# Kernel optimization log

Hardware: AMD Instinct MI355X
Metric: run time of the kernel (lower is better)

Reference implementation:

```python
import jax, jax.numpy as jnp
import numpy as np
import math

H = 512       # hidden_dim
NL = 4        # num_layers
N2 = 32       # d_state // 2
B, L = 8, 4096
DT_MIN, DT_MAX = 1e-3, 1e-1
EPS = 1e-5


def _layer_norm(x, gamma, beta):
    mu = jnp.mean(x, axis=-1, keepdims=True)
    var = jnp.mean(jnp.square(x - mu), axis=-1, keepdims=True)
    return (x - mu) * jax.lax.rsqrt(var + EPS) * gamma + beta


def setup_inputs() -> dict:
    key = jax.random.key(0)
    ks = jax.random.split(key, 8)
    x = jax.random.normal(ks[0], (B, L, H), dtype=jnp.float32)
    # S4DKernel buffers / params, stacked over layers
    log_dt = jax.random.uniform(ks[1], (NL, H)) * (math.log(DT_MAX) - math.log(DT_MIN)) + math.log(DT_MIN)
    A_imag = jnp.broadcast_to(math.pi * jnp.arange(N2, dtype=jnp.float32), (NL, H, N2)).copy()
    log_A_real = jnp.full((NL, H, N2), math.log(0.5), dtype=jnp.float32)
    C = jax.random.normal(ks[2], (NL, H, N2, 2), dtype=jnp.float32)  # view_as_real of cfloat
    D = jax.random.normal(ks[3], (NL, H), dtype=jnp.float32)
    # 1x1 Conv1d h -> 2h (pointwise linear over channels)
    W = jax.random.normal(ks[4], (NL, 2 * H, H), dtype=jnp.float32) / math.sqrt(H)
    b = jax.random.normal(ks[5], (NL, 2 * H), dtype=jnp.float32) * 0.01
    gamma = jnp.ones((NL, H), dtype=jnp.float32)
    beta = jnp.zeros((NL, H), dtype=jnp.float32)
    return dict(x=x, log_dt=log_dt, A_imag=A_imag, log_A_real=log_A_real,
                C=C, D=D, W=W, b=b, gamma=gamma, beta=beta)


def reference(x, log_dt, A_imag, log_A_real, C, D, W, b, gamma, beta):
    Bsz, Lseq, h = x.shape
    t = jnp.arange(Lseq, dtype=jnp.float32)
    for i in range(NL):
        # --- S4D kernel generation ---
        dt = jnp.exp(log_dt[i])                                    # (h,)
        Cc = C[i, ..., 0] + 1j * C[i, ..., 1]                      # (h, n)
        A = -jnp.exp(log_A_real[i]) + 1j * A_imag[i]               # (h, n)
        dA = A * dt[:, None]                                       # (h, n)
        Cmod = Cc * (jnp.exp(dA) - 1.0) / A                        # (h, n)
        # Vandermonde: exp(dA * l), reduced over state dim
        K = 2.0 * jnp.einsum('hn,hnl->hl', Cmod,
                             jnp.exp(dA[:, :, None] * t)).real     # (h, L)
        # --- FFT long convolution ---
        u = jnp.transpose(x, (0, 2, 1))                            # (B, h, L)
        kf = jnp.fft.rfft(K, n=2 * Lseq)                           # (h, L+1)
        uf = jnp.fft.rfft(u, n=2 * Lseq)                           # (B, h, L+1)
        y = jnp.fft.irfft(uf * kf, n=2 * Lseq)[..., :Lseq]         # (B, h, L)
        y = y + u * D[i][:, None]
        y = jax.nn.gelu(y, approximate=False)                      # torch nn.GELU default (erf)
        # 1x1 conv h -> 2h then GLU over channel dim
        z = jnp.einsum('oh,bhl->bol', W[i], y) + b[i][None, :, None]
        a, g = jnp.split(z, 2, axis=1)
        y = a * jax.nn.sigmoid(g)                                  # (B, h, L)
        y = jnp.transpose(y, (0, 2, 1))                            # (B, L, h)
        x = _layer_norm(y + x, gamma[i], beta[i])
    return x
```

## Files before the change

kernel.cpp:

```cpp
#include <hip/hip_runtime.h>
#include <hip/hip_bf16.h>
#include <math.h>

#define H 512
#define NL 4
#define N2 32
#define Bsz 8
#define Lseq 4096
#define BT (Bsz*Lseq)
#define LC2 64
#define NCC (BT/LC2)
#define CPB (Lseq/LC2)

typedef __attribute__((ext_vector_type(8))) short short8;
typedef __attribute__((ext_vector_type(4))) float float4v;


__device__ __forceinline__ float bf2f(unsigned short u) {
    union { unsigned int i; float f; } x; x.i = ((unsigned int)u) << 16; return x.f;
}
__device__ __forceinline__ unsigned short f2bf(float f) {
    union { float f; unsigned int i; } x; x.f = f;
    unsigned int u = x.i + 0x7fff + ((x.i >> 16) & 1);
    return (unsigned short)(u >> 16);
}
__device__ __forceinline__ uint2 pack4bf(float a, float b, float c, float d) {
    uint2 r;
    r.x = (unsigned)f2bf(a) | ((unsigned)f2bf(b) << 16);
    r.y = (unsigned)f2bf(c) | ((unsigned)f2bf(d) << 16);
    return r;
}
__device__ __forceinline__ void async_copy16(const void* g, void* l) {
    __builtin_amdgcn_global_load_lds(
        (const __attribute__((address_space(1))) void*)g,
        (__attribute__((address_space(3))) void*)l, 16, 0, 0);
}

__global__ void wconv_kernel(const float* __restrict__ W, unsigned short* __restrict__ Wbf) {
    int tid = blockIdx.x * 256 + threadIdx.x;
    Wbf[tid] = f2bf(W[tid]);
}

__global__ void params_kernel(const float* __restrict__ log_dt, const float* __restrict__ A_imag,
                              const float* __restrict__ log_A_real, const float* __restrict__ Cin,
                              float* __restrict__ dA, float* __restrict__ Ct) {
    int tid = blockIdx.x * 256 + threadIdx.x;
    int h = tid % H;
    int n = (tid / H) % N2;
    int layer = tid / (H * N2);
    float dt = expf(log_dt[layer * H + h]);
    int pidx = (layer * H + h) * N2 + n;
    float Are = -expf(log_A_real[pidx]);
    float Aim = A_imag[pidx];
    float dre = Are * dt, dim = Aim * dt;
    float er = expf(dre);
    float lre = er * cosf(dim), lim = er * sinf(dim);
    float nre = lre - 1.0f, nim = lim;
    float inv = 1.0f / (Are * Are + Aim * Aim);
    float tre = (nre * Are + nim * Aim) * inv;
    float tim = (nim * Are - nre * Aim) * inv;
    float Ccre = Cin[pidx * 2], Ccim = Cin[pidx * 2 + 1];
    int oidx = ((layer * N2 + n) * 2) * H + h;
    dA[oidx] = dre;  dA[oidx + H] = dim;
    Ct[oidx] = 2.0f * (Ccre * tre - Ccim * tim);
    Ct[oidx + H] = 2.0f * (Ccre * tim + Ccim * tre);
}

__global__ void kergen_k_kernel(const float* __restrict__ dA, const float* __restrict__ Ct,
                                unsigned short* __restrict__ kmat) {
    int t = blockIdx.x * 256 + threadIdx.x;
    int d = t & 63;
    int h = (t >> 6) & (H - 1);
    int layer = t >> 15;
    float fd = (float)d;
    float sum = 0.f;
    for (int n = 0; n < N2; n++) {
        int base = ((layer * N2 + n) * 2) * H + h;
        float dre = dA[base], dim = dA[base + H];
        float Ctr = Ct[base], Cti = Ct[base + H];
        float e = expf(dre * fd);
        sum += Ctr * e * cosf(dim * fd) - Cti * e * sinf(dim * fd);
    }
    kmat[t] = f2bf(sum);
}

__global__ void kergenW_kernel(const float* __restrict__ dA, unsigned short* __restrict__ Wst, int layer) {
    int t = blockIdx.x * 256 + threadIdx.x;
    int j = t & 63;
    int r = (t >> 6) & 63;
    int h = t >> 12;
    int n = r >> 1;
    int base = ((layer * N2 + n) * 2) * H + h;
    float dre = dA[base], dim = dA[base + H];
    float p = (float)(63 - j);
    float e = expf(dre * p);
    Wst[t] = f2bf((r & 1) ? e * sinf(dim * p) : e * cosf(dim * p));
}

__global__ void kergenV_kernel(const float* __restrict__ dA, const float* __restrict__ Ct,
                               unsigned short* __restrict__ Vl, int layer) {
    int t = blockIdx.x * 256 + threadIdx.x;
    int c2 = t & 63;
    int l = (t >> 6) & 63;
    int h = t >> 12;
    int n = c2 >> 1;
    int base = ((layer * N2 + n) * 2) * H + h;
    float dre = dA[base], dim = dA[base + H];
    float Ctr = Ct[base], Cti = Ct[base + H];
    float q = (float)(l + 1);
    float e = expf(dre * q);
    float ar = e * cosf(dim * q), ai = e * sinf(dim * q);
    float vre = Ctr * ar - Cti * ai;
    float vim = Ctr * ai + Cti * ar;
    Vl[t] = f2bf((c2 & 1) ? -vim : vre);
}

__global__ __launch_bounds__(256) void t1_f32_kernel(const float* __restrict__ xi,
                                                     unsigned short* __restrict__ ut) {
    __shared__ float tile[64][68];
    int bx = blockIdx.x;
    int pt = bx & 511, ht = bx >> 9;
    int p0 = pt * 64, h0 = ht * 64;
    int t = threadIdx.x;
    int jr = t & 15, ib = t >> 4;
#pragma unroll
    for (int pass = 0; pass < 4; pass++) {
        int i = ib + pass * 16;
        float4 v = *(const float4*)(xi + (size_t)(p0 + i) * H + h0 + jr * 4);
        *(float4*)(&tile[i][jr * 4]) = v;
    }
    __syncthreads();
#pragma unroll
    for (int pass = 0; pass < 4; pass++) {
        int i2 = ib + pass * 16;
        int j2 = jr * 4;
        uint2 pk = pack4bf(tile[j2][i2], tile[j2 + 1][i2], tile[j2 + 2][i2], tile[j2 + 3][i2]);
        *(uint2*)(ut + (size_t)(h0 + i2) * BT + p0 + j2) = pk;
    }
}

__global__ __launch_bounds__(256) void ssm_kernel(const unsigned short* __restrict__ ut,
                                                  const unsigned short* __restrict__ kmat,
                                                  const unsigned short* __restrict__ Wst,
                                                  const unsigned short* __restrict__ Vl,
                                                  const float* __restrict__ dA,
                                                  const float* __restrict__ Dp,
                                                  unsigned short* __restrict__ yt, int layer) {
    __shared__ unsigned short T[64][72];
    __shared__ unsigned short Sl[64][72];
    __shared__ unsigned short El[64][72];
    int h = blockIdx.x, b = blockIdx.y;
    int t = threadIdx.x;
    const unsigned short* km = kmat + ((size_t)layer * H + h) * 64;
    {
        int l = t >> 2, j0 = (t & 3) * 16;
#pragma unroll
        for (int g = 0; g < 2; g++) {
            short8 v;
#pragma unroll
            for (int e = 0; e < 8; e++) {
                int j = j0 + g * 8 + e;
                v[e] = (j <= l) ? (short)km[l - j] : (short)0;
            }
            *reinterpret_cast<short8*>(&T[l][j0 + g * 8]) = v;
        }
    }
    int wave = t >> 6, lane = t & 63;
    int r16 = lane & 15, quad = lane >> 4;
    const unsigned short* uh = ut + (size_t)h * BT + (size_t)b * Lseq;
    const unsigned short* wh = Wst + (size_t)h * 64 * 64;
    const unsigned short* vh = Vl + (size_t)h * 64 * 64;

    {
        int cc0 = wave * 16;
        float4v acc[4] = {};
#pragma unroll
        for (int k0 = 0; k0 < 64; k0 += 32) {
            short8 bf = *reinterpret_cast<const short8*>(uh + (size_t)(cc0 + r16) * 64 + k0 + quad * 8);
#pragma unroll
            for (int mt = 0; mt < 4; mt++) {
                short8 af = *reinterpret_cast<const short8*>(wh + (mt * 16 + r16) * 64 + k0 + quad * 8);
                acc[mt] = __builtin_amdgcn_mfma_f32_16x16x32_bf16(af, bf, acc[mt], 0, 0, 0);
            }
        }
        int cc = cc0 + r16;
#pragma unroll
        for (int mt = 0; mt < 4; mt++) {
            uint2 pk = pack4bf(acc[mt][0], acc[mt][1], acc[mt][2], acc[mt][3]);
            *(uint2*)(&Sl[cc][mt * 16 + quad * 4]) = pk;
        }
    }
    __syncthreads();

    if (wave == 0) {
        int r = lane;
        int n = r >> 1;
        int base = ((layer * N2 + n) * 2) * H + h;
        float dre = dA[base], dim = dA[base + H];
        float e = expf(dre * 64.f);
        float Lr = e * cosf(dim * 64.f), Li = e * sinf(dim * 64.f);
        float Ls = (r & 1) ? Li : -Li;
        float s = 0.f;
        for (int c = 0; c < 64; c++) {
            El[c][r] = f2bf(s);
            float p = bf2f(Sl[c][r]);
            float sp = __shfl_xor(s, 1);
            s = fmaf(Lr, s, fmaf(Ls, sp, p));
        }
    }
    __syncthreads();

    {
        int cc0 = wave * 16;
        float4v acc[4] = {};
#pragma unroll
        for (int k0 = 0; k0 < 64; k0 += 32) {
            short8 bf = *reinterpret_cast<const short8*>(uh + (size_t)(cc0 + r16) * 64 + k0 + quad * 8);
#pragma unroll
            for (int mt = 0; mt < 4; mt++) {
                short8 af = *reinterpret_cast<const short8*>(&T[mt * 16 + r16][k0 + quad * 8]);
                acc[mt] = __builtin_amdgcn_mfma_f32_16x16x32_bf16(af, bf, acc[mt], 0, 0, 0);
            }
        }
#pragma unroll
        for (int k0 = 0; k0 < 64; k0 += 32) {
            short8 bf = *reinterpret_cast<const short8*>(&El[cc0 + r16][k0 + quad * 8]);
#pragma unroll
            for (int mt = 0; mt < 4; mt++) {
                short8 af = *reinterpret_cast<const short8*>(vh + (mt * 16 + r16) * 64 + k0 + quad * 8);
                acc[mt] = __builtin_amdgcn_mfma_f32_16x16x32_bf16(af, bf, acc[mt], 0, 0, 0);
            }
        }
        float Dh = Dp[layer * H + h];
        int cc = cc0 + r16;
        unsigned short* yh = yt + (size_t)h * BT + (size_t)b * Lseq;
#pragma unroll
        for (int mt = 0; mt < 4; mt++) {
            size_t p = (size_t)cc * 64 + mt * 16 + quad * 4;
            ushort4 uu = *(const ushort4*)(uh + p);
            float o[4];
#pragma unroll
            for (int r = 0; r < 4; r++) {
                float y = acc[mt][r] + Dh * bf2f(((const unsigned short*)&uu)[r]);
                o[r] = 0.5f * y * (1.0f + erff(y * 0.70710678118654752f));
            }
            *(uint2*)(yh + p) = pack4bf(o[0], o[1], o[2], o[3]);
        }
    }
}

__global__ __launch_bounds__(256) void transpose2_kernel(const unsigned short* __restrict__ yt,
                                                         unsigned short* __restrict__ yb) {
    __shared__ unsigned short tile[64][72];
    int bx = blockIdx.x;
    int pt = bx & 511, ht = bx >> 9;
    int p0 = pt * 64, h0 = ht * 64;
    int t = threadIdx.x;
    int jr = t & 7, ib = t >> 3;
#pragma unroll
    for (int pass = 0; pass < 2; pass++) {
        int i = ib + pass * 32;
        short8 v = *reinterpret_cast<const short8*>(yt + (size_t)(h0 + i) * BT + p0 + jr * 8);
        *reinterpret_cast<short8*>(&tile[i][jr * 8]) = v;
    }
    __syncthreads();
    int pp = t >> 2, hg = t & 3;
    short8 o0, o1;
#pragma unroll
    for (int r = 0; r < 8; r++) o0[r] = (short)tile[hg * 16 + r][pp];
#pragma unroll
    for (int r = 0; r < 8; r++) o1[r] = (short)tile[hg * 16 + 8 + r][pp];
    unsigned short* dst = yb + (size_t)(p0 + pp) * H + h0 + hg * 16;
    *reinterpret_cast<short8*>(dst) = o0;
    *reinterpret_cast<short8*>(dst + 8) = o1;
}

__global__ __launch_bounds__(256) void gemm_glu_kernel(const unsigned short* __restrict__ ybf,
                                                       const unsigned short* __restrict__ Wbf,
                                                       const float* __restrict__ bias,
                                                       unsigned short* __restrict__ yo, int layer) {
    __shared__ unsigned short As[3][128 * 32];
    __shared__ unsigned short Bs[3][128 * 32];
    int tid = threadIdx.x;
    int wave = tid >> 6, lane = tid & 63;
    int wr = wave >> 1, wc = wave & 1;
    int r16 = lane & 15, quad = lane >> 4;
    int m0 = blockIdx.x * 128;
    int o0 = blockIdx.y * 64;
    const unsigned short* Wl = Wbf + (size_t)layer * 2 * H * H;

    int srow = lane >> 2;
    int scol = ((lane & 3) ^ ((srow >> 1) & 3)) * 8;
    const unsigned short* aS0 = ybf + ((size_t)(m0 + wave * 16 + srow)) * H + scol;
    const unsigned short* aS1 = aS0 + (size_t)64 * H;
    const unsigned short* bSA = Wl + ((size_t)(o0 + wave * 16 + srow)) * H + scol;
    const unsigned short* bSG = bSA + (size_t)512 * H;
    const int aoff0 = (wave * 16) * 32;
    const int aoff1 = (64 + wave * 16) * 32;

    int rcol = (quad ^ ((r16 >> 1) & 3)) * 8;

    float4v acc_a[4][2] = {}, acc_g[4][2] = {};

    async_copy16(aS0,      &As[0][aoff0]);
    async_copy16(aS1,      &As[0][aoff1]);
    async_copy16(bSA,      &Bs[0][aoff0]);
    async_copy16(bSG,      &Bs[0][aoff1]);
    async_copy16(aS0 + 32, &As[1][aoff0]);
    async_copy16(aS1 + 32, &As[1][aoff1]);
    async_copy16(bSA + 32, &Bs[1][aoff0]);
    async_copy16(bSG + 32, &Bs[1][aoff1]);
    asm volatile("s_waitcnt vmcnt(4)" ::: "memory");
    __builtin_amdgcn_s_barrier();

#pragma unroll
    for (int ks = 0; ks < 16; ++ks) {
        const int b = ks % 3;
        if (ks < 14) {
            const int nb = (ks + 2) % 3;
            const int kn = (ks + 2) * 32;
            async_copy16(aS0 + kn, &As[nb][aoff0]);
            async_copy16(aS1 + kn, &As[nb][aoff1]);
            async_copy16(bSA + kn, &Bs[nb][aoff0]);
            async_copy16(bSG + kn, &Bs[nb][aoff1]);
        }

        short8 af[4], ba[2], bg[2];
#pragma unroll
        for (int mi = 0; mi < 4; mi++)
            af[mi] = *reinterpret_cast<const short8*>(&As[b][(wr * 64 + mi * 16 + r16) * 32 + rcol]);
#pragma unroll
        for (int ni = 0; ni < 2; ni++) {
            ba[ni] = *reinterpret_cast<const short8*>(&Bs[b][(wc * 32 + ni * 16 + r16) * 32 + rcol]);
            bg[ni] = *reinterpret_cast<const short8*>(&Bs[b][(64 + wc * 32 + ni * 16 + r16) * 32 + rcol]);
        }
#pragma unroll
        for (int mi = 0; mi < 4; mi++)
#pragma unroll
            for (int ni = 0; ni < 2; ni++) {
                acc_a[mi][ni] = __builtin_amdgcn_mfma_f32_16x16x32_bf16(af[mi], ba[ni], acc_a[mi][ni], 0, 0, 0);
                acc_g[mi][ni] = __builtin_amdgcn_mfma_f32_16x16x32_bf16(af[mi], bg[ni], acc_g[mi][ni], 0, 0, 0);
            }

        if (ks < 14) {
            asm volatile("s_waitcnt vmcnt(4) lgkmcnt(0)" ::: "memory");
            __builtin_amdgcn_s_barrier();
        } else if (ks == 14) {
            asm volatile("s_waitcnt vmcnt(0) lgkmcnt(0)" ::: "memory");
            __builtin_amdgcn_s_barrier();
        }
    }

    const float* bl = bias + layer * 2 * H;
#pragma unroll
    for (int ni = 0; ni < 2; ni++) {
        int o = o0 + wc * 32 + ni * 16 + r16;
        float ba_ = bl[o], bg_ = bl[H + o];
#pragma unroll
        for (int mi = 0; mi < 4; mi++)
#pragma unroll
            for (int r = 0; r < 4; r++) {
                int l = m0 + wr * 64 + mi * 16 + quad * 4 + r;
                float av = acc_a[mi][ni][r] + ba_;
                float gv = acc_g[mi][ni][r] + bg_;
                yo[(size_t)l * H + o] = f2bf(av * (1.0f / (1.0f + expf(-gv))));
            }
    }
}

__global__ __launch_bounds__(256) void ln_t_kernel(const unsigned short* __restrict__ yo,
                                                   const float* __restrict__ xf,
                                                   const unsigned short* __restrict__ xb,
                                                   const float* __restrict__ gamma,
                                                   const float* __restrict__ beta,
                                                   unsigned short* __restrict__ xR,
                                                   unsigned short* __restrict__ ut,
                                                   int in_f32, int layer) {
    __shared__ unsigned short tl[64][520];
    int t = threadIdx.x;
    int p0 = blockIdx.x * 64;
    int lane8 = t & 7;
    int rowb = t >> 3;
    const float* gl = gamma + layer * H;
    const float* bl = beta + layer * H;
#pragma unroll
    for (int rr = 0; rr < 2; rr++) {
        int row = rowb + rr * 32;
        size_t gbase = (size_t)(p0 + row) * H;
        float v[64];
        float s = 0.f, s2 = 0.f;
#pragma unroll
        for (int cc = 0; cc < 8; cc++) {
            int h0 = (lane8 + cc * 8) * 8;
            short8 yv = *reinterpret_cast<const short8*>(yo + gbase + h0);
            if (in_f32) {
                float4 x0 = *(const float4*)(xf + gbase + h0);
                float4 x1 = *(const float4*)(xf + gbase + h0 + 4);
                v[cc * 8 + 0] = bf2f((unsigned short)yv[0]) + x0.x;
                v[cc * 8 + 1] = bf2f((unsigned short)yv[1]) + x0.y;
                v[cc * 8 + 2] = bf2f((unsigned short)yv[2]) + x0.z;
                v[cc * 8 + 3] = bf2f((unsigned short)yv[3]) + x0.w;
                v[cc * 8 + 4] = bf2f((unsigned short)yv[4]) + x1.x;
                v[cc * 8 + 5] = bf2f((unsigned short)yv[5]) + x1.y;
                v[cc * 8 + 6] = bf2f((unsigned short)yv[6]) + x1.z;
                v[cc * 8 + 7] = bf2f((unsigned short)yv[7]) + x1.w;
            } else {
                short8 xv = *reinterpret_cast<const short8*>(xb + gbase + h0);
#pragma unroll
                for (int i = 0; i < 8; i++)
                    v[cc * 8 + i] = bf2f((unsigned short)yv[i]) + bf2f((unsigned short)xv[i]);
            }
#pragma unroll
            for (int i = 0; i < 8; i++) { s += v[cc * 8 + i]; s2 = fmaf(v[cc * 8 + i], v[cc * 8 + i], s2); }
        }
        s += __shfl_xor(s, 1);  s2 += __shfl_xor(s2, 1);
        s += __shfl_xor(s, 2);  s2 += __shfl_xor(s2, 2);
        s += __shfl_xor(s, 4);  s2 += __shfl_xor(s2, 4);
        float mu = s * (1.0f / H);
        float var = s2 * (1.0f / H) - mu * mu;
        float inv = rsqrtf(var + 1e-5f);
#pragma unroll
        for (int cc = 0; cc < 8; cc++) {
            int h0 = (lane8 + cc * 8) * 8;
            float4 g0 = *(const float4*)(gl + h0);
            float4 g1 = *(const float4*)(gl + h0 + 4);
            float4 b0 = *(const float4*)(bl + h0);
            float4 b1 = *(const float4*)(bl + h0 + 4);
            short8 pk;
            pk[0] = (short)f2bf((v[cc * 8 + 0] - mu) * inv * g0.x + b0.x);
            pk[1] = (short)f2bf((v[cc * 8 + 1] - mu) * inv * g0.y + b0.y);
            pk[2] = (short)f2bf((v[cc * 8 + 2] - mu) * inv * g0.z + b0.z);
            pk[3] = (short)f2bf((v[cc * 8 + 3] - mu) * inv * g0.w + b0.w);
            pk[4] = (short)f2bf((v[cc * 8 + 4] - mu) * inv * g1.x + b1.x);
            pk[5] = (short)f2bf((v[cc * 8 + 5] - mu) * inv * g1.y + b1.y);
            pk[6] = (short)f2bf((v[cc * 8 + 6] - mu) * inv * g1.z + b1.z);
            pk[7] = (short)f2bf((v[cc * 8 + 7] - mu) * inv * g1.w + b1.w);
            *reinterpret_cast<short8*>(xR + gbase + h0) = pk;
            *reinterpret_cast<short8*>(&tl[row][h0]) = pk;
        }
    }
    __syncthreads();
#pragma unroll
    for (int hh = 0; hh < 2; hh++) {
        int h = t + hh * 256;
        unsigned short* dst = ut + (size_t)h * BT + p0;
#pragma unroll
        for (int pc = 0; pc < 8; pc++) {
            short8 o;
#pragma unroll
            for (int e = 0; e < 8; e++) o[e] = (short)tl[pc * 8 + e][h];
            *reinterpret_cast<short8*>(dst + pc * 8) = o;
        }
    }
}

__global__ __launch_bounds__(256) void ln_kernel(const unsigned short* __restrict__ yo,
                                                 const float* __restrict__ xf,
                                                 const unsigned short* __restrict__ xb,
                                                 const float* __restrict__ gamma, const float* __restrict__ beta,
                                                 float* __restrict__ of, unsigned short* __restrict__ ob,
                                                 int in_f32, int out_f32, int layer) {
    int wave = threadIdx.x >> 6, lane = threadIdx.x & 63;
    size_t row = (size_t)blockIdx.x * 4 + wave;
    const unsigned short* yp = yo + row * H + lane * 8;
    short8 yv = *reinterpret_cast<const short8*>(yp);
    float v[8];
    if (in_f32) {
        const float* xp = xf + row * H + lane * 8;
        float4 x0 = *(const float4*)(xp);
        float4 x1 = *(const float4*)(xp + 4);
        v[0] = bf2f((unsigned short)yv[0]) + x0.x; v[1] = bf2f((unsigned short)yv[1]) + x0.y;
        v[2] = bf2f((unsigned short)yv[2]) + x0.z; v[3] = bf2f((unsigned short)yv[3]) + x0.w;
        v[4] = bf2f((unsigned short)yv[4]) + x1.x; v[5] = bf2f((unsigned short)yv[5]) + x1.y;
        v[6] = bf2f((unsigned short)yv[6]) + x1.z; v[7] = bf2f((unsigned short)yv[7]) + x1.w;
    } else {
        const unsigned short* xp = xb + row * H + lane * 8;
        short8 xv = *reinterpret_cast<const short8*>(xp);
#pragma unroll
        for (int i = 0; i < 8; i++)
            v[i] = bf2f((unsigned short)yv[i]) + bf2f((unsigned short)xv[i]);
    }
    float s = 0.f, s2 = 0.f;
#pragma unroll
    for (int i = 0; i < 8; i++) { s += v[i]; s2 = fmaf(v[i], v[i], s2); }
#pragma unroll
    for (int off = 32; off; off >>= 1) {
        s += __shfl_xor(s, off);
        s2 += __shfl_xor(s2, off);
    }
    float mu = s * (1.0f / H);
    float var = s2 * (1.0f / H) - mu * mu;
    float inv = rsqrtf(var + 1e-5f);
    const float* gl = gamma + layer * H + lane * 8;
    const float* bl = beta + layer * H + lane * 8;
    float o[8];
#pragma unroll
    for (int i = 0; i < 8; i++)
        o[i] = (v[i] - mu) * inv * gl[i] + bl[i];
    if (out_f32) {
        float* op = of + row * H + lane * 8;
        *(float4*)(op) = make_float4(o[0], o[1], o[2], o[3]);
        *(float4*)(op + 4) = make_float4(o[4], o[5], o[6], o[7]);
    } else {
        unsigned short* op = ob + row * H + lane * 8;
        uint2 p0 = pack4bf(o[0], o[1], o[2], o[3]);
        uint2 p1 = pack4bf(o[4], o[5], o[6], o[7]);
        *(uint2*)(op) = p0;
        *(uint2*)(op + 4) = p1;
    }
}

extern "C" void kernel_launch(void* const* d_in, const int* in_sizes, int n_in,
                              void* d_out, int out_size, void* d_ws, size_t ws_size,
                              hipStream_t stream) {
    const float* x          = (const float*)d_in[0];
    const float* log_dt     = (const float*)d_in[1];
    const float* A_imag     = (const float*)d_in[2];
    const float* log_A_real = (const float*)d_in[3];
    const float* C          = (const float*)d_in[4];
    const float* D          = (const float*)d_in[5];
    const float* W          = (const float*)d_in[6];
    const float* bias       = (const float*)d_in[7];
    const float* gamma      = (const float*)d_in[8];
    const float* beta       = (const float*)d_in[9];

    char* ws = (char*)d_ws;
    unsigned short* xR   = (unsigned short*)(ws + 0);
    unsigned short* Vbuf = (unsigned short*)(ws + 67108864);
    unsigned short* u_t  = (unsigned short*)(ws + 100663296);
    unsigned short* ybf  = (unsigned short*)(ws + 100663296);
    unsigned short* y_t  = (unsigned short*)(ws + 134217728);
    unsigned short* yo   = (unsigned short*)(ws + 134217728);
    unsigned short* Wbf  = (unsigned short*)(ws + 167772160);
    unsigned short* Wstb = (unsigned short*)(ws + 171966464);
    unsigned short* kmat = (unsigned short*)(ws + 176160768);
    float*          dA   = (float*)(ws + 176422912);
    float*          Ct   = (float*)(ws + 176947200);
    float* xout_final    = (float*)d_out;

    wconv_kernel<<<NL * 2 * H * H / 256, 256, 0, stream>>>(W, Wbf);
    params_kernel<<<NL * N2 * H / 256, 256, 0, stream>>>(log_dt, A_imag, log_A_real, C, dA, Ct);
    kergen_k_kernel<<<NL * H * 64 / 256, 256, 0, stream>>>(dA, Ct, kmat);

    for (int layer = 0; layer < NL; ++layer) {
        if (layer == 0)
            t1_f32_kernel<<<4096, 256, 0, stream>>>(x, u_t);
        kergenW_kernel<<<H * 64 * 64 / 256, 256, 0, stream>>>(dA, Wstb, layer);
        kergenV_kernel<<<H * 64 * 64 / 256, 256, 0, stream>>>(dA, Ct, Vbuf, layer);
        ssm_kernel<<<dim3(H, Bsz), 256, 0, stream>>>(u_t, kmat, Wstb, Vbuf, dA, D, y_t, layer);
        transpose2_kernel<<<4096, 256, 0, stream>>>(y_t, ybf);
        gemm_glu_kernel<<<dim3(BT / 128, H / 64), 256, 0, stream>>>(ybf, Wbf, bias, yo, layer);
        if (layer < NL - 1) {
            ln_t_kernel<<<BT / 64, 256, 0, stream>>>(yo, x, xR, gamma, beta,
                                                     xR, u_t, (layer == 0) ? 1 : 0, layer);
        } else {
            ln_kernel<<<BT / 4, 256, 0, stream>>>(yo, x, xR, gamma, beta,
                                                  xout_final, xR, 0, 1, layer);
        }
    }
}
```

Baseline: 841.3 us.

## Parallelize inter-chunk state scan across all four waves with two-level scan

The sequential 64-step complex state recurrence was run by a single wave while the other three sat idle. Now each wave scans 16 chunks locally and publishes its end state to shared memory. Each wave then combines the preceding waves' totals using the 16-step power of the decay and adds the propagated carry times per-step powers to its local states. The result is written in place into Sl, which removes the separate El buffer. This shortens the serial critical path but adds extra transcendental work, an extra barrier, and possibly different rounding from the recomputed powers.

```diff
diff --git a/kernel.cpp b/kernel.cpp
--- a/kernel.cpp
+++ b/kernel.cpp
@@ -148,7 +148,7 @@
                                                   unsigned short* __restrict__ yt, int layer) {
     __shared__ unsigned short T[64][72];
     __shared__ unsigned short Sl[64][72];
-    __shared__ unsigned short El[64][72];
+    __shared__ float Tw[4][64];
     int h = blockIdx.x, b = blockIdx.y;
     int t = threadIdx.x;
     const unsigned short* km = kmat + ((size_t)layer * H + h) * 64;
@@ -192,20 +192,49 @@
     }
     __syncthreads();
 
-    if (wave == 0) {
+    {
         int r = lane;
         int n = r >> 1;
         int base = ((layer * N2 + n) * 2) * H + h;
         float dre = dA[base], dim = dA[base + H];
-        float e = expf(dre * 64.f);
-        float Lr = e * cosf(dim * 64.f), Li = e * sinf(dim * 64.f);
+        float e1 = expf(dre * 64.f);
+        float Lr = e1 * cosf(dim * 64.f), Li = e1 * sinf(dim * 64.f);
         float Ls = (r & 1) ? Li : -Li;
+        int c0 = wave * 16;
+
+        float eloc[16];
         float s = 0.f;
-        for (int c = 0; c < 64; c++) {
-            El[c][r] = f2bf(s);
-            float p = bf2f(Sl[c][r]);
+#pragma unroll
+        for (int k = 0; k < 16; k++) {
+            float p = bf2f(Sl[c0 + k][r]);
+            eloc[k] = s;
             float sp = __shfl_xor(s, 1);
             s = fmaf(Lr, s, fmaf(Ls, sp, p));
+        }
+        Tw[wave][r] = s;
+        __syncthreads();
+
+        float e16 = expf(dre * 1024.f);
+        float Lr16 = e16 * cosf(dim * 1024.f), Li16 = e16 * sinf(dim * 1024.f);
+        float Ls16 = (r & 1) ? Li16 : -Li16;
+        float C = 0.f;
+        for (int j = 0; j < wave; j++) {
+            float Tj = Tw[j][r];
+            float Cp = __shfl_xor(C, 1);
+            C = fmaf(Lr16, C, fmaf(Ls16, Cp, Tj));
+        }
+        float cpp = __shfl_xor(C, 1);
+
+        float pw = (r & 1) ? 0.f : 1.f;
+#pragma unroll
+        for (int k = 0; k < 16; k++) {
+            float pp = __shfl_xor(pw, 1);
+            float u1 = (r & 1) ? pp : pw;
+            float u2 = (r & 1) ? pw : pp;
+            float tt = u2 * cpp;
+            float ead = fmaf(u1, C, (r & 1) ? tt : -tt);
+            Sl[c0 + k][r] = f2bf(eloc[k] + ead);
+            pw = fmaf(Lr, pw, Ls * pp);
         }
     }
     __syncthreads();
@@ -224,7 +253,7 @@
         }
 #pragma unroll
         for (int k0 = 0; k0 < 64; k0 += 32) {
-            short8 bf = *reinterpret_cast<const short8*>(&El[cc0 + r16][k0 + quad * 8]);
+            short8 bf = *reinterpret_cast<const short8*>(&Sl[cc0 + r16][k0 + quad * 8]);
 #pragma unroll
             for (int mt = 0; mt < 4; mt++) {
                 short8 af = *reinterpret_cast<const short8*>(vh + (mt * 16 + r16) * 64 + k0 + quad * 8);
```

Result: no change. 838.2 us (-0.4%).
